# Optimization experiments

Measured on AMD Instinct MI355X. Metric: run time of the kernel, lower is better.

Reference implementation:

```python
import jax, jax.numpy as jnp
import numpy as np

N = 2_000_000   # n_nodes
D = 8           # manifold_dim
C = 1.0         # hyperbolic curvature

# ---- Poincare ball ops (curvature C), vectorized over leading node axis ----
def _hyp_proj(x, eps=1e-5):
    norm = jnp.linalg.norm(x, axis=-1, keepdims=True)
    max_norm = (1.0 - eps) / jnp.sqrt(C)
    return jnp.where(norm > max_norm, x / norm * max_norm, x)

def _mobius_add(x, y):
    xy = jnp.sum(x * y, axis=-1, keepdims=True)
    nx = jnp.sum(x ** 2, axis=-1, keepdims=True)
    ny = jnp.sum(y ** 2, axis=-1, keepdims=True)
    num = (1.0 + 2.0 * C * xy + C * ny) * x + (1.0 - C * nx) * y
    den = 1.0 + 2.0 * C * xy + C ** 2 * nx * ny
    return num / (den + 1e-10)

def _hyp_exp(x, v):
    nv = jnp.maximum(jnp.linalg.norm(v, axis=-1, keepdims=True), 1e-10)
    sc = jnp.sqrt(C)
    nx = jnp.linalg.norm(x, axis=-1, keepdims=True)
    lam = 2.0 / (1.0 - C * nx ** 2)
    coef = jnp.tanh(sc * lam * nv / 2) / (sc * nv)
    return _hyp_proj(_mobius_add(x, coef * v))

def _hyp_log(x, y):
    sub = _mobius_add(-x, y)
    ns = jnp.maximum(jnp.linalg.norm(sub, axis=-1, keepdims=True), 1e-10)
    sc = jnp.sqrt(C)
    nx = jnp.linalg.norm(x, axis=-1, keepdims=True)
    lam = 2.0 / (1.0 - C * nx ** 2)
    coef = jnp.arctanh(sc * ns) / (sc * ns * lam / 2)
    return coef * sub

# ---- sphere ops ----
def _sph_proj(x):
    return x / (jnp.linalg.norm(x, axis=-1, keepdims=True) + 1e-10)

def _sph_log(x, y):
    xy = jnp.clip(jnp.sum(x * y, axis=-1, keepdims=True), -1.0 + 1e-6, 1.0 - 1e-6)
    coef = jnp.arccos(xy) / jnp.sqrt(1.0 - xy ** 2 + 1e-10)
    return coef * (y - xy * x)

def _sph_exp(x, v):
    nv = jnp.maximum(jnp.linalg.norm(v, axis=-1, keepdims=True), 1e-10)
    return _sph_proj(jnp.cos(nv) * x + jnp.sin(nv) * v / nv)


def setup_inputs() -> dict:
    key = jax.random.key(0)
    ks = jax.random.split(key, 9)
    f32 = jnp.float32
    return {
        'features': jax.random.normal(ks[0], (N, 8), dtype=f32),
        # flax Dense default init ~ lecun_normal: std = 1/sqrt(fan_in)
        'W_hyp': jax.random.normal(ks[1], (2, D), dtype=f32) / np.sqrt(2.0),
        'b_hyp': jnp.zeros((D,), dtype=f32),
        'W_spd': jax.random.normal(ks[2], (3, 3), dtype=f32) / np.sqrt(3.0),
        'b_spd': jnp.zeros((3,), dtype=f32),
        'W_sph': jax.random.normal(ks[3], (2, D), dtype=f32) / np.sqrt(2.0),
        'b_sph': jnp.zeros((D,), dtype=f32),
        'W_int': jax.random.normal(ks[4], (4 + D + 3 + D, 32), dtype=f32) / np.sqrt(4.0 + D + 3 + D),
        'b_int': jnp.zeros((32,), dtype=f32),
    }


def reference(features, W_hyp, b_hyp, W_spd, b_spd, W_sph, b_sph, W_int, b_int):
    euclid = features[:, :4]            # [N,4]
    mf = features[:, 4:]                # [N,4] manifold features

    # --- hyperbolic branch: exp-map of MLP output at the origin ---
    hyp_tan = mf[:, 0:2] @ W_hyp + b_hyp            # [N,D]
    hyp_pt = _hyp_exp(jnp.zeros_like(hyp_tan), hyp_tan)

    # --- SPD branch: matrices are diag(exp(Dense(feat)) + 0.1) ---
    spd_diag = jnp.exp(mf[:, 0:3] @ W_spd + b_spd) + 0.1   # [N,3]

    # --- sphere branch ---
    sph_pt = _sph_proj(mf[:, 2:4] @ W_sph + b_sph)          # [N,D]

    # --- geodesic refinement: hyperbolic ---
    hc = _hyp_proj(jnp.mean(hyp_pt, axis=0, keepdims=True))
    hyp_ref = _hyp_exp(hyp_pt, 0.1 * _hyp_log(hyp_pt, hc))

    # --- geodesic refinement: SPD ---
    # matrices and centroid are diagonal, so (1-a)*M + a*centroid is diagonal;
    # eigh + clamp + reconstruct of a diagonal SPD matrix == diag(max(d, 1e-6))
    geo_mean = jnp.exp(jnp.mean(jnp.log(spd_diag + 1e-8), axis=0))   # [3]
    spd_ref_diag = jnp.maximum(0.9 * spd_diag + 0.1 * geo_mean, 1e-6)  # [N,3]
    spd_ref = jnp.eye(3, dtype=spd_ref_diag.dtype) * spd_ref_diag[:, None, :]  # [N,3,3]

    # --- geodesic refinement: sphere ---
    sc = _sph_proj(jnp.mean(sph_pt, axis=0, keepdims=True))
    sph_ref = _sph_exp(sph_pt, 0.1 * _sph_log(sph_pt, sc))

    # --- pullbacks to tangent space + integration ---
    hyp_pull = _hyp_log(jnp.zeros_like(hyp_ref), hyp_ref)
    spd_pull = jnp.log(spd_ref_diag + 1e-8)
    combined = jnp.concatenate([euclid, hyp_pull, spd_pull, sph_ref], axis=-1)  # [N,23]
    integrated = jax.nn.relu(combined @ W_int + b_int)    # [N,32]
    return (integrated, hyp_ref, spd_ref, sph_ref, combined)
```

## Files before the change

kernel.cpp:

```cpp
#include <hip/hip_runtime.h>
#include <math.h>

#define NB1 1024
#define BS  256

__device__ __forceinline__ void compute_base(
    const float4 mf,
    const float* __restrict__ Wh, const float* __restrict__ bh,
    const float* __restrict__ Ws, const float* __restrict__ bs,
    const float* __restrict__ Wp, const float* __restrict__ bp,
    float* hp, float* sd, float* sp)
{
    float ht[8];
    float nv2 = 0.f;
#pragma unroll
    for (int j = 0; j < 8; ++j) {
        float t = mf.x * Wh[j] + mf.y * Wh[8 + j] + bh[j];
        ht[j] = t; nv2 += t * t;
    }
    float nv = fmaxf(sqrtf(nv2), 1e-10f);
    float coef = tanhf(nv) / nv;
    float pn2 = 0.f;
#pragma unroll
    for (int j = 0; j < 8; ++j) {
        float p = coef * ht[j];
        hp[j] = p; pn2 += p * p;
    }
    float pn = sqrtf(pn2);
    if (pn > 0.99999f) {
        float s = 0.99999f / pn;
#pragma unroll
        for (int j = 0; j < 8; ++j) hp[j] *= s;
    }
#pragma unroll
    for (int k = 0; k < 3; ++k) {
        float t = mf.x * Ws[k] + mf.y * Ws[3 + k] + mf.z * Ws[6 + k] + bs[k];
        sd[k] = expf(t) + 0.1f;
    }
    float sl[8]; float sn2 = 0.f;
#pragma unroll
    for (int j = 0; j < 8; ++j) {
        float t = mf.z * Wp[j] + mf.w * Wp[8 + j] + bp[j];
        sl[j] = t; sn2 += t * t;
    }
    float isn = 1.0f / (sqrtf(sn2) + 1e-10f);
#pragma unroll
    for (int j = 0; j < 8; ++j) sp[j] = sl[j] * isn;
}

__global__ __launch_bounds__(BS) void reduce_kernel(
    const float* __restrict__ feat, int n,
    const float* __restrict__ Wh, const float* __restrict__ bh,
    const float* __restrict__ Ws, const float* __restrict__ bs,
    const float* __restrict__ Wp, const float* __restrict__ bp,
    float* __restrict__ partials)
{
    float acc[19];
#pragma unroll
    for (int i = 0; i < 19; ++i) acc[i] = 0.f;
    int stride = gridDim.x * blockDim.x;
    for (int row = blockIdx.x * blockDim.x + threadIdx.x; row < n; row += stride) {
        float4 mf = *(const float4*)(feat + (size_t)row * 8 + 4);
        float hp[8], sd[3], sp[8];
        compute_base(mf, Wh, bh, Ws, bs, Wp, bp, hp, sd, sp);
#pragma unroll
        for (int j = 0; j < 8; ++j) acc[j] += hp[j];
#pragma unroll
        for (int k = 0; k < 3; ++k) acc[8 + k] += logf(sd[k] + 1e-8f);
#pragma unroll
        for (int j = 0; j < 8; ++j) acc[11 + j] += sp[j];
    }
#pragma unroll
    for (int i = 0; i < 19; ++i) {
#pragma unroll
        for (int off = 32; off >= 1; off >>= 1)
            acc[i] += __shfl_down(acc[i], off, 64);
    }
    __shared__ float red[4][19];
    int lane = threadIdx.x & 63, wid = threadIdx.x >> 6;
    if (lane == 0) {
#pragma unroll
        for (int i = 0; i < 19; ++i) red[wid][i] = acc[i];
    }
    __syncthreads();
    if (threadIdx.x < 19) {
        float s = red[0][threadIdx.x] + red[1][threadIdx.x] +
                  red[2][threadIdx.x] + red[3][threadIdx.x];
        partials[(size_t)blockIdx.x * 19 + threadIdx.x] = s;
    }
}

__global__ void finalize_kernel(const float* __restrict__ partials,
                                float* __restrict__ cons, int n)
{
    __shared__ double ms[19];
    int tid = threadIdx.x;
    int k = tid >> 3, w = tid & 7;
    if (k < 19) {
        double s = 0.0;
        for (int b = w; b < NB1; b += 8) s += (double)partials[(size_t)b * 19 + k];
#pragma unroll
        for (int off = 4; off >= 1; off >>= 1) s += __shfl_down(s, off, 8);
        if (w == 0) ms[k] = s / (double)n;
    }
    __syncthreads();
    if (tid == 0) {
        double hn2 = 0.0;
        for (int j = 0; j < 8; ++j) hn2 += ms[j] * ms[j];
        double hn = sqrt(hn2);
        double sch = (hn > 0.99999) ? (0.99999 / hn) : 1.0;
        for (int j = 0; j < 8; ++j) cons[j] = (float)(ms[j] * sch);
        for (int kk = 0; kk < 3; ++kk) cons[8 + kk] = (float)exp(ms[8 + kk]);
        double sn2 = 0.0;
        for (int j = 0; j < 8; ++j) sn2 += ms[11 + j] * ms[11 + j];
        double sn = sqrt(sn2) + 1e-10;
        for (int j = 0; j < 8; ++j) cons[11 + j] = (float)(ms[11 + j] / sn);
    }
}

__global__ __launch_bounds__(BS) void main_kernel(
    const float* __restrict__ feat, int n,
    const float* __restrict__ Wh, const float* __restrict__ bh,
    const float* __restrict__ Ws, const float* __restrict__ bs,
    const float* __restrict__ Wp, const float* __restrict__ bp,
    const float* __restrict__ cons,
    const float* __restrict__ Wi, const float* __restrict__ bi,
    float* __restrict__ out)
{
    __shared__ float sbuf[BS * 33];
    const int tid = threadIdx.x;
    const int blockStart = blockIdx.x * BS;
    const int row = blockStart + tid;
    const bool valid = row < n;
    const int vr = min(BS, n - blockStart);

    float* out_int = out;
    float* out_hyp = out + (size_t)n * 32;
    float* out_spd = out + (size_t)n * 40;
    float* out_sph = out + (size_t)n * 49;
    float* out_cmb = out + (size_t)n * 57;

    float comb[23], hr[8], srd[3], sr[8];

    if (valid) {
        size_t r = (size_t)row;
        float4 eu = *(const float4*)(feat + r * 8);
        float4 mf = *(const float4*)(feat + r * 8 + 4);

        float p[8], sd[3], sp[8];
        compute_base(mf, Wh, bh, Ws, bs, Wp, bp, p, sd, sp);

        float hc[8];
#pragma unroll
        for (int j = 0; j < 8; ++j) hc[j] = cons[j];
        float nx2 = 0.f;
#pragma unroll
        for (int j = 0; j < 8; ++j) nx2 += p[j] * p[j];
        float xy = 0.f, ny2 = 0.f;
#pragma unroll
        for (int j = 0; j < 8; ++j) { xy -= p[j] * hc[j]; ny2 += hc[j] * hc[j]; }
        float a1 = 1.f + 2.f * xy + ny2;
        float b1 = 1.f - nx2;
        float id1 = 1.f / (1.f + 2.f * xy + nx2 * ny2 + 1e-10f);
        float sub[8]; float ns2 = 0.f;
#pragma unroll
        for (int j = 0; j < 8; ++j) {
            float s = (a1 * (-p[j]) + b1 * hc[j]) * id1;
            sub[j] = s; ns2 += s * s;
        }
        float ns  = fmaxf(sqrtf(ns2), 1e-10f);
        float lam = 2.f / (1.f - nx2);
        float vcoef = 0.1f * atanhf(ns) / (ns * lam * 0.5f);
        float v[8]; float nv2 = 0.f;
#pragma unroll
        for (int j = 0; j < 8; ++j) { float t = vcoef * sub[j]; v[j] = t; nv2 += t * t; }
        float nvv = fmaxf(sqrtf(nv2), 1e-10f);
        float ecoef = tanhf(lam * nvv * 0.5f) / nvv;
        float y[8]; float xy2 = 0.f, nyy2 = 0.f;
#pragma unroll
        for (int j = 0; j < 8; ++j) { float t = ecoef * v[j]; y[j] = t; xy2 += p[j] * t; nyy2 += t * t; }
        float a2 = 1.f + 2.f * xy2 + nyy2;
        float b2 = 1.f - nx2;
        float id2 = 1.f / (1.f + 2.f * xy2 + nx2 * nyy2 + 1e-10f);
        float hn2 = 0.f;
#pragma unroll
        for (int j = 0; j < 8; ++j) { float t = (a2 * p[j] + b2 * y[j]) * id2; hr[j] = t; hn2 += t * t; }
        float hn = sqrtf(hn2);
        if (hn > 0.99999f) {
            float s = 0.99999f / hn;
#pragma unroll
            for (int j = 0; j < 8; ++j) hr[j] *= s;
        }
        float nsb2 = 0.f;
#pragma unroll
        for (int j = 0; j < 8; ++j) nsb2 += hr[j] * hr[j];
        float nsb = fmaxf(sqrtf(nsb2), 1e-10f);
        float pcoef = atanhf(nsb) / nsb;

        float scv[8], geo3[3];
#pragma unroll
        for (int j = 0; j < 8; ++j) scv[j] = cons[11 + j];
#pragma unroll
        for (int k = 0; k < 3; ++k) geo3[k] = cons[8 + k];
        float sxy = 0.f;
#pragma unroll
        for (int j = 0; j < 8; ++j) sxy += sp[j] * scv[j];
        sxy = fminf(fmaxf(sxy, -1.f + 1e-6f), 1.f - 1e-6f);
        float svcoef = 0.1f * acosf(sxy) / sqrtf(1.f - sxy * sxy + 1e-10f);
        float sv[8]; float snv2 = 0.f;
#pragma unroll
        for (int j = 0; j < 8; ++j) { float t = svcoef * (scv[j] - sxy * sp[j]); sv[j] = t; snv2 += t * t; }
        float snv = fmaxf(sqrtf(snv2), 1e-10f);
        float cn  = cosf(snv);
        float sn_ = sinf(snv) / snv;
        float st[8]; float stn2 = 0.f;
#pragma unroll
        for (int j = 0; j < 8; ++j) { float t = cn * sp[j] + sn_ * sv[j]; st[j] = t; stn2 += t * t; }
        float istn = 1.f / (sqrtf(stn2) + 1e-10f);
#pragma unroll
        for (int j = 0; j < 8; ++j) sr[j] = st[j] * istn;

#pragma unroll
        for (int k = 0; k < 3; ++k)
            srd[k] = fmaxf(0.9f * sd[k] + 0.1f * geo3[k], 1e-6f);

        comb[0] = eu.x; comb[1] = eu.y; comb[2] = eu.z; comb[3] = eu.w;
#pragma unroll
        for (int j = 0; j < 8; ++j) comb[4 + j] = pcoef * hr[j];
#pragma unroll
        for (int k = 0; k < 3; ++k) comb[12 + k] = logf(srd[k] + 1e-8f);
#pragma unroll
        for (int j = 0; j < 8; ++j) comb[15 + j] = sr[j];
    }

    if (valid) {
        float* lrow = sbuf + tid * 33;
#pragma unroll
        for (int j = 0; j < 32; ++j) {
            float acc = bi[j];
#pragma unroll
            for (int k2 = 0; k2 < 23; ++k2) acc += comb[k2] * Wi[k2 * 32 + j];
            lrow[j] = fmaxf(acc, 0.f);
        }
    }
    __syncthreads();
    {
        float* dst = out_int + (size_t)blockStart * 32;
        const int E = vr * 32;
        for (int i = tid; i < E; i += BS) dst[i] = sbuf[(i >> 5) * 33 + (i & 31)];
    }
    __syncthreads();

    if (valid) {
        float* lrow = sbuf + tid * 23;
#pragma unroll
        for (int k = 0; k < 23; ++k) lrow[k] = comb[k];
    }
    __syncthreads();
    {
        float* dst = out_cmb + (size_t)blockStart * 23;
        const int E = vr * 23;
        for (int i = tid; i < E; i += BS) dst[i] = sbuf[i];
    }
    __syncthreads();

    if (valid) {
        float* ls = sbuf + tid * 9;
        ls[0] = srd[0]; ls[1] = 0.f;    ls[2] = 0.f;
        ls[3] = 0.f;    ls[4] = srd[1]; ls[5] = 0.f;
        ls[6] = 0.f;    ls[7] = 0.f;    ls[8] = srd[2];
        float* lh = sbuf + BS * 9 + tid * 9;
#pragma unroll
        for (int j = 0; j < 8; ++j) lh[j] = hr[j];
        float* lp = sbuf + 2 * BS * 9 + tid * 9;
#pragma unroll
        for (int j = 0; j < 8; ++j) lp[j] = sr[j];
    }
    __syncthreads();
    {
        float* d1 = out_spd + (size_t)blockStart * 9;
        int E = vr * 9;
        for (int i = tid; i < E; i += BS) d1[i] = sbuf[i];
        float* d2 = out_hyp + (size_t)blockStart * 8;
        E = vr * 8;
        for (int i = tid; i < E; i += BS) d2[i] = sbuf[BS * 9 + (i >> 3) * 9 + (i & 7)];
        float* d3 = out_sph + (size_t)blockStart * 8;
        for (int i = tid; i < E; i += BS) d3[i] = sbuf[2 * BS * 9 + (i >> 3) * 9 + (i & 7)];
    }
}

extern "C" void kernel_launch(void* const* d_in, const int* in_sizes, int n_in,
                              void* d_out, int out_size, void* d_ws, size_t ws_size,
                              hipStream_t stream) {
    const float* feat = (const float*)d_in[0];
    const float* Wh = (const float*)d_in[1];
    const float* bh = (const float*)d_in[2];
    const float* Ws = (const float*)d_in[3];
    const float* bs = (const float*)d_in[4];
    const float* Wp = (const float*)d_in[5];
    const float* bp = (const float*)d_in[6];
    const float* Wi = (const float*)d_in[7];
    const float* bi = (const float*)d_in[8];
    int n = in_sizes[0] / 8;

    float* partials = (float*)d_ws;
    float* cons = partials + NB1 * 19;
    float* out = (float*)d_out;

    reduce_kernel<<<NB1, BS, 0, stream>>>(feat, n, Wh, bh, Ws, bs, Wp, bp, partials);
    finalize_kernel<<<1, 256, 0, stream>>>(partials, cons, n);
    main_kernel<<<(n + BS - 1) / BS, BS, 0, stream>>>(feat, n, Wh, bh, Ws, bs, Wp, bp,
                                                      cons, Wi, bi, out);
}
```

Baseline: 735.9 us.

## Vectorize output stores with nontemporal float4 writes and stage Wi in LDS

Output writes for each segment now use 128-bit nontemporal stores, reading from a reorganized padded float4 shared-memory layout that avoids bank conflicts. Before this, every segment was written as scalar floats. The integration weights and bias are loaded into LDS once per block, which adds an extra barrier. The goal is fewer store instructions and less cache pollution in a kernel bound by write bandwidth. The float4 paths rely on blockStart*23 and blockStart*9 being 16-byte aligned, which holds because BS is 256.

```diff
diff --git a/kernel.cpp b/kernel.cpp
--- a/kernel.cpp
+++ b/kernel.cpp
@@ -3,6 +3,15 @@
 
 #define NB1 1024
 #define BS  256
+
+typedef float f4v __attribute__((ext_vector_type(4)));
+
+__device__ __forceinline__ void nts4(float4* p, float4 v) {
+    __builtin_nontemporal_store(*(const f4v*)&v, (f4v*)p);
+}
+__device__ __forceinline__ void nts1(float* p, float v) {
+    __builtin_nontemporal_store(v, p);
+}
 
 __device__ __forceinline__ void compute_base(
     const float4 mf,
@@ -127,12 +136,20 @@
     const float* __restrict__ Wi, const float* __restrict__ bi,
     float* __restrict__ out)
 {
-    __shared__ float sbuf[BS * 33];
+    __shared__ float4 sbuf4[8 * 257];
+    __shared__ float  swi[736];
+    __shared__ float  sbi[32];
+    float* sf = (float*)sbuf4;
+
     const int tid = threadIdx.x;
     const int blockStart = blockIdx.x * BS;
     const int row = blockStart + tid;
     const bool valid = row < n;
     const int vr = min(BS, n - blockStart);
+
+    for (int i = tid; i < 184; i += BS)
+        ((float4*)swi)[i] = ((const float4*)Wi)[i];
+    if (tid < 8) ((float4*)sbi)[tid] = ((const float4*)bi)[tid];
 
     float* out_int = out;
     float* out_hyp = out + (size_t)n * 32;
@@ -233,26 +250,34 @@
         for (int j = 0; j < 8; ++j) comb[15 + j] = sr[j];
     }
 
+    __syncthreads();
+
     if (valid) {
-        float* lrow = sbuf + tid * 33;
-#pragma unroll
-        for (int j = 0; j < 32; ++j) {
-            float acc = bi[j];
-#pragma unroll
-            for (int k2 = 0; k2 < 23; ++k2) acc += comb[k2] * Wi[k2 * 32 + j];
-            lrow[j] = fmaxf(acc, 0.f);
+#pragma unroll
+        for (int c4 = 0; c4 < 8; ++c4) {
+            float a_[4];
+#pragma unroll
+            for (int jj = 0; jj < 4; ++jj) {
+                int j = c4 * 4 + jj;
+                float acc = sbi[j];
+#pragma unroll
+                for (int k2 = 0; k2 < 23; ++k2) acc += comb[k2] * swi[k2 * 32 + j];
+                a_[jj] = fmaxf(acc, 0.f);
+            }
+            sbuf4[c4 * 257 + tid] = make_float4(a_[0], a_[1], a_[2], a_[3]);
         }
     }
     __syncthreads();
     {
-        float* dst = out_int + (size_t)blockStart * 32;
-        const int E = vr * 32;
-        for (int i = tid; i < E; i += BS) dst[i] = sbuf[(i >> 5) * 33 + (i & 31)];
+        float4* dst4 = (float4*)(out_int + (size_t)blockStart * 32);
+        const int E4 = vr * 8;
+        for (int i4 = tid; i4 < E4; i4 += BS)
+            nts4(dst4 + i4, sbuf4[(i4 & 7) * 257 + (i4 >> 3)]);
     }
     __syncthreads();
 
     if (valid) {
-        float* lrow = sbuf + tid * 23;
+        float* lrow = sf + tid * 23;
 #pragma unroll
         for (int k = 0; k < 23; ++k) lrow[k] = comb[k];
     }
@@ -260,32 +285,44 @@
     {
         float* dst = out_cmb + (size_t)blockStart * 23;
         const int E = vr * 23;
-        for (int i = tid; i < E; i += BS) dst[i] = sbuf[i];
+        const int E4 = E >> 2;
+        float4* dst4 = (float4*)dst;
+        for (int i4 = tid; i4 < E4; i4 += BS)
+            nts4(dst4 + i4, ((const float4*)sf)[i4]);
+        for (int i = (E4 << 2) + tid; i < E; i += BS)
+            nts1(dst + i, sf[i]);
     }
     __syncthreads();
 
     if (valid) {
-        float* ls = sbuf + tid * 9;
+        float* ls = sf + tid * 9;
         ls[0] = srd[0]; ls[1] = 0.f;    ls[2] = 0.f;
         ls[3] = 0.f;    ls[4] = srd[1]; ls[5] = 0.f;
         ls[6] = 0.f;    ls[7] = 0.f;    ls[8] = srd[2];
-        float* lh = sbuf + BS * 9 + tid * 9;
-#pragma unroll
-        for (int j = 0; j < 8; ++j) lh[j] = hr[j];
-        float* lp = sbuf + 2 * BS * 9 + tid * 9;
-#pragma unroll
-        for (int j = 0; j < 8; ++j) lp[j] = sr[j];
+        sbuf4[576 + 0 * 257 + tid]  = make_float4(hr[0], hr[1], hr[2], hr[3]);
+        sbuf4[576 + 1 * 257 + tid]  = make_float4(hr[4], hr[5], hr[6], hr[7]);
+        sbuf4[1090 + 0 * 257 + tid] = make_float4(sr[0], sr[1], sr[2], sr[3]);
+        sbuf4[1090 + 1 * 257 + tid] = make_float4(sr[4], sr[5], sr[6], sr[7]);
     }
     __syncthreads();
     {
         float* d1 = out_spd + (size_t)blockStart * 9;
-        int E = vr * 9;
-        for (int i = tid; i < E; i += BS) d1[i] = sbuf[i];
-        float* d2 = out_hyp + (size_t)blockStart * 8;
-        E = vr * 8;
-        for (int i = tid; i < E; i += BS) d2[i] = sbuf[BS * 9 + (i >> 3) * 9 + (i & 7)];
-        float* d3 = out_sph + (size_t)blockStart * 8;
-        for (int i = tid; i < E; i += BS) d3[i] = sbuf[2 * BS * 9 + (i >> 3) * 9 + (i & 7)];
+        const int E = vr * 9;
+        const int E4 = E >> 2;
+        float4* d14 = (float4*)d1;
+        for (int i4 = tid; i4 < E4; i4 += BS)
+            nts4(d14 + i4, ((const float4*)sf)[i4]);
+        for (int i = (E4 << 2) + tid; i < E; i += BS)
+            nts1(d1 + i, sf[i]);
+
+        float4* d24 = (float4*)(out_hyp + (size_t)blockStart * 8);
+        const int H4 = vr * 2;
+        for (int i4 = tid; i4 < H4; i4 += BS)
+            nts4(d24 + i4, sbuf4[576 + (i4 & 1) * 257 + (i4 >> 1)]);
+
+        float4* d34 = (float4*)(out_sph + (size_t)blockStart * 8);
+        for (int i4 = tid; i4 < H4; i4 += BS)
+            nts4(d34 + i4, sbuf4[1090 + (i4 & 1) * 257 + (i4 >> 1)]);
     }
 }
 
```

After: 712.5 us. 1.03x faster.
